# Optimization experiments

Measured on AMD Instinct MI355X. Metric: run time of the kernel, lower is better.

## Reference

```python
import jax, jax.numpy as jnp
import numpy as np

H = 40  # HIDDEN_SIZE


def _gru_layer(x_tbi, Wih, Whh, bih, bhh):
    """PyTorch-convention GRU layer. x_tbi: (T, B, I). Returns (ys (T,B,H), h_T (B,H)).
    Gate order in stacked weights is (r, z, n) as in torch.nn.GRU:
      r = sigmoid(W_ir x + b_ir + W_hr h + b_hr)
      z = sigmoid(W_iz x + b_iz + W_hz h + b_hz)
      n = tanh(W_in x + b_in + r * (W_hn h + b_hn))
      h' = (1 - z) * n + z * h
    """
    # Precompute all input projections in one big GEMM: (T,B,3H)
    xg = jnp.einsum('tbi,gi->tbg', x_tbi, Wih) + bih
    B = x_tbi.shape[1]
    h0 = jnp.zeros((B, H), x_tbi.dtype)

    def step(h, xg_t):
        hg = h @ Whh.T + bhh                       # (B, 3H)
        xr, xz, xn = jnp.split(xg_t, 3, axis=-1)
        hr, hz, hn = jnp.split(hg, 3, axis=-1)
        r = jax.nn.sigmoid(xr + hr)
        z = jax.nn.sigmoid(xz + hz)
        n = jnp.tanh(xn + r * hn)
        h_new = (1.0 - z) * n + z * h
        return h_new, h_new

    hT, ys = jax.lax.scan(step, h0, xg)
    return ys, hT


def setup_inputs() -> dict:
    key = jax.random.key(0)
    ks = jax.random.split(key, 9)
    B, T, I = 4096, 256, 16
    s = 1.0 / np.sqrt(H)  # torch GRU init: U(-1/sqrt(H), 1/sqrt(H))
    u = lambda k, shape: jax.random.uniform(k, shape, jnp.float32, -s, s)
    return {
        "x": jax.random.normal(ks[0], (B, T, I), jnp.float32),
        "Wih0": u(ks[1], (3 * H, I)),
        "Whh0": u(ks[2], (3 * H, H)),
        "bih0": u(ks[3], (3 * H,)),
        "bhh0": u(ks[4], (3 * H,)),
        "Wih1": u(ks[5], (3 * H, H)),
        "Whh1": u(ks[6], (3 * H, H)),
        "bih1": u(ks[7], (3 * H,)),
        "bhh1": u(ks[8], (3 * H,)),
    }


def reference(x, Wih0, Whh0, bih0, bhh0, Wih1, Whh1, bih1, bhh1):
    # batch_first input (B,T,I) -> time-major (T,B,I) for scan
    x_tbi = jnp.transpose(x, (1, 0, 2))
    y0, _ = _gru_layer(x_tbi, Wih0, Whh0, bih0, bhh0)   # layer 0 full sequence
    _, hT = _gru_layer(y0, Wih1, Whh1, bih1, bhh1)      # layer 1 final state
    return hT  # (B, H) == h[-1]
```

## Files before the change

### kernel.cpp

```cpp
#include <hip/hip_runtime.h>

#define T_STEPS 256
#define HID 40
#define EPB 16
#define NTHR 512
#define RR 56
#define PP (16 * RR)
#define OL1 (2 * PP)
#define STOT (4 * PP)

typedef __attribute__((ext_vector_type(8))) short bf16x8;
typedef __attribute__((ext_vector_type(4))) float f32x4;
typedef __attribute__((ext_vector_type(8))) float f32x8;
typedef __attribute__((ext_vector_type(4))) unsigned int u32x4;

__device__ __forceinline__ unsigned short bf16_rne(float v) {
    unsigned int x = __float_as_uint(v);
    unsigned int r = x + 0x7FFFu + ((x >> 16) & 1u);
    return (unsigned short)(r >> 16);
}
__device__ __forceinline__ unsigned short bf16_cvt(float v) {
    unsigned int r;
    asm("v_cvt_pk_bf16_f32 %0, %1, %2" : "=v"(r) : "v"(v), "v"(v));
    return (unsigned short)r;
}
__device__ __forceinline__ float sigm(float v) {
    return __builtin_amdgcn_rcpf(1.0f + __builtin_amdgcn_exp2f(-1.4426950408889634f * v));
}
__device__ __forceinline__ float tanh_f(float v) {
    return 1.0f - 2.0f * __builtin_amdgcn_rcpf(__builtin_amdgcn_exp2f(2.8853900817779268f * v) + 1.0f);
}

#define MF(A_, B_, C_) C_ = __builtin_amdgcn_mfma_f32_16x16x32_bf16(A_, B_, C_, 0, 0, 0)
#define PINV(v) asm volatile("" : "+v"(v))

__device__ bf16x8 afrag(const float* Whh, const float* Wih, int KX,
                        int rh, int rx, int c, int qrow) {
    bf16x8 f;
    #pragma unroll
    for (int j = 0; j < 8; ++j) f[j] = 0;
    #pragma unroll
    for (int j = 0; j < 8; ++j) {
        const int k = 32 * c + qrow * 8 + j;
        if (k < 40) {
            if (rh >= 0) f[j] = (short)bf16_rne(Whh[rh * 40 + k]);
        } else if (k < 40 + KX) {
            if (rx >= 0) f[j] = (short)bf16_rne(Wih[rx * KX + (k - 40)]);
        }
    }
    return f;
}

__global__ __launch_bounds__(NTHR, 2)
void gru2_kernel(const float* __restrict__ x,
                 const float* __restrict__ Wih0, const float* __restrict__ Whh0,
                 const float* __restrict__ bih0, const float* __restrict__ bhh0,
                 const float* __restrict__ Wih1, const float* __restrict__ Whh1,
                 const float* __restrict__ bih1, const float* __restrict__ bhh1,
                 float* __restrict__ out)
{
    __shared__ __align__(16) unsigned short S[STOT];

    const int tid  = threadIdx.x;
    const int wid  = tid >> 6;
    const int l    = tid & 63;
    const int col  = l & 15;
    const int qrow = l >> 4;
    const int ps   = (l & 15) & 3;
    const int pu   = (l & 15) >> 2;
    const int e0   = blockIdx.x * EPB;

    const bool isL1 = wid >= 4;
    const int  m    = isL1 ? wid - 4 : wid;
    const int  NTIL = (m < 2) ? 3 : 2;
    const int  Tb   = (m < 2) ? 3 * m : 6 + 2 * (m - 2);

    const float* Whh = isL1 ? Whh1 : Whh0;
    const float* Wih = isL1 ? Wih1 : Wih0;
    const float* bih = isL1 ? bih1 : bih0;
    const float* bhh = isL1 ? bhh1 : bhh0;
    const int KX = isL1 ? 40 : 16;

    bf16x8 ZF;
    #pragma unroll
    for (int j = 0; j < 8; ++j) ZF[j] = 0;
    bf16x8 F00=ZF,F01=ZF,F02=ZF, F10=ZF,F11=ZF,F12=ZF, F20=ZF,F21=ZF,F22=ZF;
    f32x4 BB0, BB1, BB2;
    {
#define RRX(u, RH, RX) \
        const int RH = (ps == 2) ? -1 : (ps == 0 ? (u) : ps == 1 ? 40 + (u) : 80 + (u)); \
        const int RX = (ps == 3) ? -1 : (ps == 0 ? (u) : ps == 1 ? 40 + (u) : 80 + (u));
        {
            const int u0 = 4 * (Tb + 0) + pu;
            RRX(u0, rh0, rx0);
            F00 = afrag(Whh, Wih, KX, rh0, rx0, 0, qrow);
            F01 = afrag(Whh, Wih, KX, rh0, rx0, 1, qrow);
            if (isL1) F02 = afrag(Whh, Wih, KX, rh0, rx0, 2, qrow);
        }
        {
            const int u1 = 4 * (Tb + 1) + pu;
            RRX(u1, rh1, rx1);
            F10 = afrag(Whh, Wih, KX, rh1, rx1, 0, qrow);
            F11 = afrag(Whh, Wih, KX, rh1, rx1, 1, qrow);
            if (isL1) F12 = afrag(Whh, Wih, KX, rh1, rx1, 2, qrow);
        }
        if (NTIL == 3) {
            const int u2 = 4 * (Tb + 2) + pu;
            RRX(u2, rh2, rx2);
            F20 = afrag(Whh, Wih, KX, rh2, rx2, 0, qrow);
            F21 = afrag(Whh, Wih, KX, rh2, rx2, 1, qrow);
            if (isL1) F22 = afrag(Whh, Wih, KX, rh2, rx2, 2, qrow);
        }
        const int uc0 = 4 * (Tb + 0) + qrow;
        const int uc1 = 4 * (Tb + 1) + qrow;
        BB0[0] = bih[uc0] + bhh[uc0];
        BB0[1] = bih[40 + uc0] + bhh[40 + uc0];
        BB0[2] = bih[80 + uc0];
        BB0[3] = bhh[80 + uc0];
        BB1[0] = bih[uc1] + bhh[uc1];
        BB1[1] = bih[40 + uc1] + bhh[40 + uc1];
        BB1[2] = bih[80 + uc1];
        BB1[3] = bhh[80 + uc1];
        if (NTIL == 3) {
            const int uc2 = 4 * (Tb + 2) + qrow;
            BB2[0] = bih[uc2] + bhh[uc2];
            BB2[1] = bih[40 + uc2] + bhh[40 + uc2];
            BB2[2] = bih[80 + uc2];
            BB2[3] = bhh[80 + uc2];
        } else {
            BB2[0] = BB2[1] = BB2[2] = BB2[3] = 0.f;
        }
    }
    PINV(F00); PINV(F01); PINV(F02);
    PINV(F10); PINV(F11); PINV(F12);
    PINV(F20); PINV(F21); PINV(F22);
    PINV(BB0); PINV(BB1); PINV(BB2);

    int r0p0, r0p1, r1p0, r1p1, r2p0, r2p1;
    if (!isL1) {
        r0p0 = col * RR + 8 * qrow;  r0p1 = r0p0 + PP;
        r1p0 = col * RR + 32;        r1p1 = r1p0 + PP;
        r2p0 = 0;                    r2p1 = 0;
    } else {
        auto ga = [&](int g, int p) -> int {
            if (g < 5)  return OL1 + p * PP + col * RR + 8 * g;
            if (g < 10) return p * PP + col * RR + 8 * (g - 5);
            return p * PP + col * RR;
        };
        r0p0 = ga(qrow, 0);     r0p1 = ga(qrow, 1);
        r1p0 = ga(4 + qrow, 0); r1p1 = ga(4 + qrow, 1);
        r2p0 = ga(8 + qrow, 0); r2p1 = ga(8 + qrow, 1);
    }
    const int wof = (isL1 ? OL1 : 0) + col * RR + 4 * Tb + qrow;
    const bool usex = (qrow == 1) || (qrow == 2);
    unsigned short* Sb = &S[0];
    float hA0 = 0.f, hA1 = 0.f, hA2 = 0.f;

    for (int idx = tid; idx < STOT; idx += NTHR) Sb[idx] = 0;

    const float* xrow = x + (size_t)(e0 + col) * (T_STEPS * 16) + ((qrow == 2) ? 8 : 0);
    f32x8 XA, XB, XC, XD;
    #pragma unroll
    for (int j = 0; j < 8; ++j) { XA[j] = 0.f; XB[j] = 0.f; XC[j] = 0.f; XD[j] = 0.f; }
    if (!isL1) {
        XA = *(const f32x8*)(xrow);
        XB = *(const f32x8*)(xrow + 16);
        XC = *(const f32x8*)(xrow + 32);
        XD = *(const f32x8*)(xrow + 48);
    }
    __syncthreads();

#define GMATH(C, H) \
    const float r_ = sigm(C[0]); \
    const float z_ = sigm(C[1]); \
    const float n_ = tanh_f(C[2] + r_ * C[3]); \
    H = n_ + z_ * (H - n_);

#define BODY(RP, XQ) { \
    if (!isL1) { \
        const bf16x8 S0 = *(const bf16x8*)(Sb + r0p##RP); \
        bf16x8 S1 = *(const bf16x8*)(Sb + r1p##RP); \
        if (t < T_STEPS) { \
            unsigned int xw0, xw1, xw2, xw3; \
            asm("v_cvt_pk_bf16_f32 %0, %1, %2" : "=v"(xw0) : "v"(XQ[0]), "v"(XQ[1])); \
            asm("v_cvt_pk_bf16_f32 %0, %1, %2" : "=v"(xw1) : "v"(XQ[2]), "v"(XQ[3])); \
            asm("v_cvt_pk_bf16_f32 %0, %1, %2" : "=v"(xw2) : "v"(XQ[4]), "v"(XQ[5])); \
            asm("v_cvt_pk_bf16_f32 %0, %1, %2" : "=v"(xw3) : "v"(XQ[6]), "v"(XQ[7])); \
            if (t + 4 < T_STEPS) XQ = *(const f32x8*)(xrow + (t + 4) * 16); \
            u32x4 s1u = *(const u32x4*)&S1; \
            s1u[0] = usex ? xw0 : s1u[0]; \
            s1u[1] = usex ? xw1 : s1u[1]; \
            s1u[2] = usex ? xw2 : s1u[2]; \
            s1u[3] = usex ? xw3 : s1u[3]; \
            S1 = *(const bf16x8*)&s1u; \
            f32x4 c0 = __builtin_amdgcn_mfma_f32_16x16x32_bf16(F00, S0, BB0, 0, 0, 0); \
            MF(F01, S1, c0); \
            f32x4 c1 = __builtin_amdgcn_mfma_f32_16x16x32_bf16(F10, S0, BB1, 0, 0, 0); \
            MF(F11, S1, c1); \
            { GMATH(c0, hA0); Sb[(1 - (RP)) * PP + wof + 0] = bf16_cvt(hA0); } \
            { GMATH(c1, hA1); Sb[(1 - (RP)) * PP + wof + 4] = bf16_cvt(hA1); } \
            if (NTIL == 3) { \
                f32x4 c2 = __builtin_amdgcn_mfma_f32_16x16x32_bf16(F20, S0, BB2, 0, 0, 0); \
                MF(F21, S1, c2); \
                GMATH(c2, hA2); Sb[(1 - (RP)) * PP + wof + 8] = bf16_cvt(hA2); \
            } \
        } \
    } else { \
        const bf16x8 S0 = *(const bf16x8*)(Sb + r0p##RP); \
        const bf16x8 S1 = *(const bf16x8*)(Sb + r1p##RP); \
        const bf16x8 S2 = *(const bf16x8*)(Sb + r2p##RP); \
        f32x4 c0 = __builtin_amdgcn_mfma_f32_16x16x32_bf16(F00, S0, BB0, 0, 0, 0); \
        MF(F01, S1, c0); MF(F02, S2, c0); \
        f32x4 c1 = __builtin_amdgcn_mfma_f32_16x16x32_bf16(F10, S0, BB1, 0, 0, 0); \
        MF(F11, S1, c1); MF(F12, S2, c1); \
        if (t > 0) { \
            { GMATH(c0, hA0); Sb[(1 - (RP)) * PP + wof + 0] = bf16_cvt(hA0); } \
            { GMATH(c1, hA1); Sb[(1 - (RP)) * PP + wof + 4] = bf16_cvt(hA1); } \
        } \
        if (NTIL == 3) { \
            f32x4 c2 = __builtin_amdgcn_mfma_f32_16x16x32_bf16(F20, S0, BB2, 0, 0, 0); \
            MF(F21, S1, c2); MF(F22, S2, c2); \
            if (t > 0) { GMATH(c2, hA2); Sb[(1 - (RP)) * PP + wof + 8] = bf16_cvt(hA2); } \
        } \
    } \
    ++t; \
    __syncthreads(); }

    int t = 0;
    #pragma unroll 1
    for (int it = 0; it < 64; ++it) {
        BODY(0, XA)
        BODY(1, XB)
        BODY(0, XC)
        BODY(1, XD)
    }
    BODY(0, XA)

    if (isL1) {
        float* op = out + (size_t)(e0 + col) * HID + 4 * Tb + qrow;
        op[0] = hA0;
        op[4] = hA1;
        if (NTIL == 3) op[8] = hA2;
    }
}

extern "C" void kernel_launch(void* const* d_in, const int* in_sizes, int n_in,
                              void* d_out, int out_size, void* d_ws, size_t ws_size,
                              hipStream_t stream) {
    const float* x    = (const float*)d_in[0];
    const float* Wih0 = (const float*)d_in[1];
    const float* Whh0 = (const float*)d_in[2];
    const float* bih0 = (const float*)d_in[3];
    const float* bhh0 = (const float*)d_in[4];
    const float* Wih1 = (const float*)d_in[5];
    const float* Whh1 = (const float*)d_in[6];
    const float* bih1 = (const float*)d_in[7];
    const float* bhh1 = (const float*)d_in[8];
    float* out = (float*)d_out;

    dim3 grid(4096 / EPB), block(NTHR);
    hipLaunchKernelGGL(gru2_kernel, grid, block, 0, stream,
                       x, Wih0, Whh0, bih0, bhh0, Wih1, Whh1, bih1, bhh1, out);
}
```

Baseline: 233.7 us.

## Split GRU step into two phases and balance tiles over ten waves

Each workgroup now runs ten waves instead of eight, five per layer, and every wave owns exactly two output tiles, so the old uneven 3/2 tile split is gone. Each timestep becomes two barrier-separated phases. In one phase layer 0 issues its MFMAs while layer 1 applies gate math to results from the previous step, and in the other phase the roles swap. The goal is to shorten the critical path per step by overlapping one layer's matrix work with the other layer's activations. The cost is a second barrier per step, a lower launch-bounds occupancy hint (1 instead of 2), and an epilogue that finishes the last layer-1 step.

```diff
diff --git a/kernel.cpp b/kernel.cpp
--- a/kernel.cpp
+++ b/kernel.cpp
@@ -3,7 +3,7 @@
 #define T_STEPS 256
 #define HID 40
 #define EPB 16
-#define NTHR 512
+#define NTHR 640
 #define RR 56
 #define PP (16 * RR)
 #define OL1 (2 * PP)
@@ -51,7 +51,7 @@
     return f;
 }
 
-__global__ __launch_bounds__(NTHR, 2)
+__global__ __launch_bounds__(NTHR, 1)
 void gru2_kernel(const float* __restrict__ x,
                  const float* __restrict__ Wih0, const float* __restrict__ Whh0,
                  const float* __restrict__ bih0, const float* __restrict__ bhh0,
@@ -70,10 +70,8 @@
     const int pu   = (l & 15) >> 2;
     const int e0   = blockIdx.x * EPB;
 
-    const bool isL1 = wid >= 4;
-    const int  m    = isL1 ? wid - 4 : wid;
-    const int  NTIL = (m < 2) ? 3 : 2;
-    const int  Tb   = (m < 2) ? 3 * m : 6 + 2 * (m - 2);
+    const bool isL1 = wid >= 5;
+    const int  m    = isL1 ? wid - 5 : wid;
 
     const float* Whh = isL1 ? Whh1 : Whh0;
     const float* Wih = isL1 ? Wih1 : Wih0;
@@ -84,35 +82,28 @@
     bf16x8 ZF;
     #pragma unroll
     for (int j = 0; j < 8; ++j) ZF[j] = 0;
-    bf16x8 F00=ZF,F01=ZF,F02=ZF, F10=ZF,F11=ZF,F12=ZF, F20=ZF,F21=ZF,F22=ZF;
-    f32x4 BB0, BB1, BB2;
+    bf16x8 F00=ZF,F01=ZF,F02=ZF, F10=ZF,F11=ZF,F12=ZF;
+    f32x4 BB0, BB1;
     {
 #define RRX(u, RH, RX) \
         const int RH = (ps == 2) ? -1 : (ps == 0 ? (u) : ps == 1 ? 40 + (u) : 80 + (u)); \
         const int RX = (ps == 3) ? -1 : (ps == 0 ? (u) : ps == 1 ? 40 + (u) : 80 + (u));
         {
-            const int u0 = 4 * (Tb + 0) + pu;
+            const int u0 = 4 * (2 * m) + pu;
             RRX(u0, rh0, rx0);
             F00 = afrag(Whh, Wih, KX, rh0, rx0, 0, qrow);
             F01 = afrag(Whh, Wih, KX, rh0, rx0, 1, qrow);
             if (isL1) F02 = afrag(Whh, Wih, KX, rh0, rx0, 2, qrow);
         }
         {
-            const int u1 = 4 * (Tb + 1) + pu;
+            const int u1 = 4 * (2 * m + 1) + pu;
             RRX(u1, rh1, rx1);
             F10 = afrag(Whh, Wih, KX, rh1, rx1, 0, qrow);
             F11 = afrag(Whh, Wih, KX, rh1, rx1, 1, qrow);
             if (isL1) F12 = afrag(Whh, Wih, KX, rh1, rx1, 2, qrow);
         }
-        if (NTIL == 3) {
-            const int u2 = 4 * (Tb + 2) + pu;
-            RRX(u2, rh2, rx2);
-            F20 = afrag(Whh, Wih, KX, rh2, rx2, 0, qrow);
-            F21 = afrag(Whh, Wih, KX, rh2, rx2, 1, qrow);
-            if (isL1) F22 = afrag(Whh, Wih, KX, rh2, rx2, 2, qrow);
-        }
-        const int uc0 = 4 * (Tb + 0) + qrow;
-        const int uc1 = 4 * (Tb + 1) + qrow;
+        const int uc0 = 8 * m + qrow;
+        const int uc1 = 8 * m + 4 + qrow;
         BB0[0] = bih[uc0] + bhh[uc0];
         BB0[1] = bih[40 + uc0] + bhh[40 + uc0];
         BB0[2] = bih[80 + uc0];
@@ -121,52 +112,44 @@
         BB1[1] = bih[40 + uc1] + bhh[40 + uc1];
         BB1[2] = bih[80 + uc1];
         BB1[3] = bhh[80 + uc1];
-        if (NTIL == 3) {
-            const int uc2 = 4 * (Tb + 2) + qrow;
-            BB2[0] = bih[uc2] + bhh[uc2];
-            BB2[1] = bih[40 + uc2] + bhh[40 + uc2];
-            BB2[2] = bih[80 + uc2];
-            BB2[3] = bhh[80 + uc2];
-        } else {
-            BB2[0] = BB2[1] = BB2[2] = BB2[3] = 0.f;
-        }
     }
     PINV(F00); PINV(F01); PINV(F02);
     PINV(F10); PINV(F11); PINV(F12);
-    PINV(F20); PINV(F21); PINV(F22);
-    PINV(BB0); PINV(BB1); PINV(BB2);
-
-    int r0p0, r0p1, r1p0, r1p1, r2p0, r2p1;
-    if (!isL1) {
-        r0p0 = col * RR + 8 * qrow;  r0p1 = r0p0 + PP;
-        r1p0 = col * RR + 32;        r1p1 = r1p0 + PP;
-        r2p0 = 0;                    r2p1 = 0;
-    } else {
-        auto ga = [&](int g, int p) -> int {
-            if (g < 5)  return OL1 + p * PP + col * RR + 8 * g;
-            if (g < 10) return p * PP + col * RR + 8 * (g - 5);
-            return p * PP + col * RR;
+    PINV(BB0); PINV(BB1);
+
+    int rd0, rd1, g0, g1, g2;
+    rd0 = col * RR + 8 * qrow;
+    rd1 = col * RR + 32;
+    {
+        auto ga = [&](int g) -> int {
+            if (g < 5)  return OL1 + col * RR + 8 * g;
+            if (g < 10) return col * RR + 8 * (g - 5);
+            return col * RR;
         };
-        r0p0 = ga(qrow, 0);     r0p1 = ga(qrow, 1);
-        r1p0 = ga(4 + qrow, 0); r1p1 = ga(4 + qrow, 1);
-        r2p0 = ga(8 + qrow, 0); r2p1 = ga(8 + qrow, 1);
-    }
-    const int wof = (isL1 ? OL1 : 0) + col * RR + 4 * Tb + qrow;
+        g0 = ga(qrow);
+        g1 = ga(4 + qrow);
+        g2 = ga(8 + qrow);
+    }
+    const int w0  = col * RR + 8 * m + qrow;
+    const int w0b = w0 + 4;
+    const int w1  = OL1 + col * RR + 8 * m + qrow;
+    const int w1b = w1 + 4;
     const bool usex = (qrow == 1) || (qrow == 2);
     unsigned short* Sb = &S[0];
-    float hA0 = 0.f, hA1 = 0.f, hA2 = 0.f;
+    float hA0 = 0.f, hA1 = 0.f;
+    f32x4 cP0, cP1;
+    cP0[0]=cP0[1]=cP0[2]=cP0[3]=0.f;
+    cP1[0]=cP1[1]=cP1[2]=cP1[3]=0.f;
 
     for (int idx = tid; idx < STOT; idx += NTHR) Sb[idx] = 0;
 
     const float* xrow = x + (size_t)(e0 + col) * (T_STEPS * 16) + ((qrow == 2) ? 8 : 0);
-    f32x8 XA, XB, XC, XD;
-    #pragma unroll
-    for (int j = 0; j < 8; ++j) { XA[j] = 0.f; XB[j] = 0.f; XC[j] = 0.f; XD[j] = 0.f; }
+    f32x8 XA, XB;
+    #pragma unroll
+    for (int j = 0; j < 8; ++j) { XA[j] = 0.f; XB[j] = 0.f; }
     if (!isL1) {
         XA = *(const f32x8*)(xrow);
         XB = *(const f32x8*)(xrow + 16);
-        XC = *(const f32x8*)(xrow + 32);
-        XD = *(const f32x8*)(xrow + 48);
     }
     __syncthreads();
 
@@ -176,71 +159,74 @@
     const float n_ = tanh_f(C[2] + r_ * C[3]); \
     H = n_ + z_ * (H - n_);
 
-#define BODY(RP, XQ) { \
+#define STEP(RP, XQ) { \
+     \
     if (!isL1) { \
-        const bf16x8 S0 = *(const bf16x8*)(Sb + r0p##RP); \
-        bf16x8 S1 = *(const bf16x8*)(Sb + r1p##RP); \
-        if (t < T_STEPS) { \
-            unsigned int xw0, xw1, xw2, xw3; \
-            asm("v_cvt_pk_bf16_f32 %0, %1, %2" : "=v"(xw0) : "v"(XQ[0]), "v"(XQ[1])); \
-            asm("v_cvt_pk_bf16_f32 %0, %1, %2" : "=v"(xw1) : "v"(XQ[2]), "v"(XQ[3])); \
-            asm("v_cvt_pk_bf16_f32 %0, %1, %2" : "=v"(xw2) : "v"(XQ[4]), "v"(XQ[5])); \
-            asm("v_cvt_pk_bf16_f32 %0, %1, %2" : "=v"(xw3) : "v"(XQ[6]), "v"(XQ[7])); \
-            if (t + 4 < T_STEPS) XQ = *(const f32x8*)(xrow + (t + 4) * 16); \
-            u32x4 s1u = *(const u32x4*)&S1; \
-            s1u[0] = usex ? xw0 : s1u[0]; \
-            s1u[1] = usex ? xw1 : s1u[1]; \
-            s1u[2] = usex ? xw2 : s1u[2]; \
-            s1u[3] = usex ? xw3 : s1u[3]; \
-            S1 = *(const bf16x8*)&s1u; \
-            f32x4 c0 = __builtin_amdgcn_mfma_f32_16x16x32_bf16(F00, S0, BB0, 0, 0, 0); \
-            MF(F01, S1, c0); \
-            f32x4 c1 = __builtin_amdgcn_mfma_f32_16x16x32_bf16(F10, S0, BB1, 0, 0, 0); \
-            MF(F11, S1, c1); \
-            { GMATH(c0, hA0); Sb[(1 - (RP)) * PP + wof + 0] = bf16_cvt(hA0); } \
-            { GMATH(c1, hA1); Sb[(1 - (RP)) * PP + wof + 4] = bf16_cvt(hA1); } \
-            if (NTIL == 3) { \
-                f32x4 c2 = __builtin_amdgcn_mfma_f32_16x16x32_bf16(F20, S0, BB2, 0, 0, 0); \
-                MF(F21, S1, c2); \
-                GMATH(c2, hA2); Sb[(1 - (RP)) * PP + wof + 8] = bf16_cvt(hA2); \
-            } \
-        } \
+        const bf16x8 S0 = *(const bf16x8*)(Sb + rd0 + (RP) * PP); \
+        bf16x8 S1 = *(const bf16x8*)(Sb + rd1 + (RP) * PP); \
+        unsigned int xw0, xw1, xw2, xw3; \
+        asm("v_cvt_pk_bf16_f32 %0, %1, %2" : "=v"(xw0) : "v"(XQ[0]), "v"(XQ[1])); \
+        asm("v_cvt_pk_bf16_f32 %0, %1, %2" : "=v"(xw1) : "v"(XQ[2]), "v"(XQ[3])); \
+        asm("v_cvt_pk_bf16_f32 %0, %1, %2" : "=v"(xw2) : "v"(XQ[4]), "v"(XQ[5])); \
+        asm("v_cvt_pk_bf16_f32 %0, %1, %2" : "=v"(xw3) : "v"(XQ[6]), "v"(XQ[7])); \
+        if (t + 2 < T_STEPS) XQ = *(const f32x8*)(xrow + (t + 2) * 16); \
+        u32x4 s1u = *(const u32x4*)&S1; \
+        s1u[0] = usex ? xw0 : s1u[0]; \
+        s1u[1] = usex ? xw1 : s1u[1]; \
+        s1u[2] = usex ? xw2 : s1u[2]; \
+        s1u[3] = usex ? xw3 : s1u[3]; \
+        S1 = *(const bf16x8*)&s1u; \
+        cA0 = __builtin_amdgcn_mfma_f32_16x16x32_bf16(F00, S0, BB0, 0, 0, 0); \
+        MF(F01, S1, cA0); \
+        cA1 = __builtin_amdgcn_mfma_f32_16x16x32_bf16(F10, S0, BB1, 0, 0, 0); \
+        MF(F11, S1, cA1); \
+    } else if (t >= 2) { \
+        { GMATH(cP0, hA0); Sb[w1  + (RP) * PP] = bf16_cvt(hA0); } \
+        { GMATH(cP1, hA1); Sb[w1b + (RP) * PP] = bf16_cvt(hA1); } \
+    } \
+    __syncthreads();   \
+     \
+    if (!isL1) { \
+        { GMATH(cA0, hA0); Sb[w0  + (1 - (RP)) * PP] = bf16_cvt(hA0); } \
+        { GMATH(cA1, hA1); Sb[w0b + (1 - (RP)) * PP] = bf16_cvt(hA1); } \
     } else { \
-        const bf16x8 S0 = *(const bf16x8*)(Sb + r0p##RP); \
-        const bf16x8 S1 = *(const bf16x8*)(Sb + r1p##RP); \
-        const bf16x8 S2 = *(const bf16x8*)(Sb + r2p##RP); \
-        f32x4 c0 = __builtin_amdgcn_mfma_f32_16x16x32_bf16(F00, S0, BB0, 0, 0, 0); \
-        MF(F01, S1, c0); MF(F02, S2, c0); \
-        f32x4 c1 = __builtin_amdgcn_mfma_f32_16x16x32_bf16(F10, S0, BB1, 0, 0, 0); \
-        MF(F11, S1, c1); MF(F12, S2, c1); \
-        if (t > 0) { \
-            { GMATH(c0, hA0); Sb[(1 - (RP)) * PP + wof + 0] = bf16_cvt(hA0); } \
-            { GMATH(c1, hA1); Sb[(1 - (RP)) * PP + wof + 4] = bf16_cvt(hA1); } \
-        } \
-        if (NTIL == 3) { \
-            f32x4 c2 = __builtin_amdgcn_mfma_f32_16x16x32_bf16(F20, S0, BB2, 0, 0, 0); \
-            MF(F21, S1, c2); MF(F22, S2, c2); \
-            if (t > 0) { GMATH(c2, hA2); Sb[(1 - (RP)) * PP + wof + 8] = bf16_cvt(hA2); } \
-        } \
+        const bf16x8 S0 = *(const bf16x8*)(Sb + g0 + (RP) * PP); \
+        const bf16x8 S1 = *(const bf16x8*)(Sb + g1 + (RP) * PP); \
+        const bf16x8 S2 = *(const bf16x8*)(Sb + g2 + (RP) * PP); \
+        cP0 = __builtin_amdgcn_mfma_f32_16x16x32_bf16(F00, S0, BB0, 0, 0, 0); \
+        MF(F01, S1, cP0); MF(F02, S2, cP0); \
+        cP1 = __builtin_amdgcn_mfma_f32_16x16x32_bf16(F10, S0, BB1, 0, 0, 0); \
+        MF(F11, S1, cP1); MF(F12, S2, cP1); \
     } \
     ++t; \
-    __syncthreads(); }
+    __syncthreads();   }
 
     int t = 0;
+    f32x4 cA0, cA1;
     #pragma unroll 1
-    for (int it = 0; it < 64; ++it) {
-        BODY(0, XA)
-        BODY(1, XB)
-        BODY(0, XC)
-        BODY(1, XD)
-    }
-    BODY(0, XA)
+    for (int it = 0; it < 128; ++it) {
+        STEP(0, XA)
+        STEP(1, XB)
+    }
 
     if (isL1) {
-        float* op = out + (size_t)(e0 + col) * HID + 4 * Tb + qrow;
+        { GMATH(cP0, hA0); Sb[w1  + 0 * PP] = bf16_cvt(hA0); }
+        { GMATH(cP1, hA1); Sb[w1b + 0 * PP] = bf16_cvt(hA1); }
+    }
+    __syncthreads();
+    if (isL1) {
+        const bf16x8 S0 = *(const bf16x8*)(Sb + g0 + 0 * PP);
+        const bf16x8 S1 = *(const bf16x8*)(Sb + g1 + 0 * PP);
+        const bf16x8 S2 = *(const bf16x8*)(Sb + g2 + 0 * PP);
+        f32x4 c0 = __builtin_amdgcn_mfma_f32_16x16x32_bf16(F00, S0, BB0, 0, 0, 0);
+        MF(F01, S1, c0); MF(F02, S2, c0);
+        f32x4 c1 = __builtin_amdgcn_mfma_f32_16x16x32_bf16(F10, S0, BB1, 0, 0, 0);
+        MF(F11, S1, c1); MF(F12, S2, c1);
+        { GMATH(c0, hA0); }
+        { GMATH(c1, hA1); }
+        float* op = out + (size_t)(e0 + col) * HID + 8 * m + qrow;
         op[0] = hA0;
         op[4] = hA1;
-        if (NTIL == 3) op[8] = hA2;
     }
 }
 
```

Result: slower. 239.0 us (+2.3%).
